# Kernel optimization log

Measured on AMD Instinct MI355X. Metric: run time of the kernel, lower is better.

## Reference

```python
import jax, jax.numpy as jnp
import numpy as np
from jax import lax

B, H, W, T, C = 2, 28, 28, 28, 192
WS = 7
NH = 6
HD = C // NH
N = WS ** 3
L = H * W * T

# static relative position index (matches torch buffer construction)
_coords = np.stack(np.meshgrid(np.arange(WS), np.arange(WS), np.arange(WS), indexing='ij'))  # (3,7,7,7)
_flat = _coords.reshape(3, -1)
_rel = (_flat[:, :, None] - _flat[:, None, :]).transpose(1, 2, 0).astype(np.int64)  # (N,N,3)
_rel[..., 0] += WS - 1; _rel[..., 1] += WS - 1; _rel[..., 2] += WS - 1
_rel[..., 0] *= (2 * WS - 1) ** 2
_rel[..., 1] *= (2 * WS - 1)
REL_IDX = jnp.asarray(_rel.sum(-1))  # (N,N)


def setup_inputs() -> dict:
    key = jax.random.key(0)
    ks = jax.random.split(key, 24)
    s = 0.02
    d = {
        'x': jax.random.normal(ks[0], (B, L, C), jnp.float32),
        'y': jax.random.normal(ks[1], (B, L, C), jnp.float32),
        'mask_matrix': jnp.zeros((64, N, N), jnp.float32),
        'norm1_g': jnp.ones((C,), jnp.float32),
        'norm1_b': jnp.zeros((C,), jnp.float32),
        'qkv_w': jax.random.normal(ks[2], (3 * C, C), jnp.float32) * s,
        'qkv_b': jnp.zeros((3 * C,), jnp.float32),
        'proj_w': jax.random.normal(ks[3], (C, C), jnp.float32) * s,
        'proj_b': jnp.zeros((C,), jnp.float32),
        'rpb_table': jax.random.normal(ks[4], ((2 * WS - 1) ** 3, NH), jnp.float32) * s,
        'norm2_g': jnp.ones((C,), jnp.float32),
        'norm2_b': jnp.zeros((C,), jnp.float32),
        'fc1_w': jax.random.normal(ks[5], (4 * C, C), jnp.float32) * s,
        'fc1_b': jnp.zeros((4 * C,), jnp.float32),
        'fc2_w': jax.random.normal(ks[6], (C, 4 * C), jnp.float32) * s,
        'fc2_b': jnp.zeros((C,), jnp.float32),
        'cab1_w': jax.random.normal(ks[7], (C // 3, C, 3, 3, 3), jnp.float32) * s,
        'cab1_b': jnp.zeros((C // 3,), jnp.float32),
        'cab2_w': jax.random.normal(ks[8], (C, C // 3, 3, 3, 3), jnp.float32) * s,
        'cab2_b': jnp.zeros((C,), jnp.float32),
        'ca1_w': jax.random.normal(ks[9], (C // 16, C), jnp.float32) * s,
        'ca1_b': jnp.zeros((C // 16,), jnp.float32),
        'ca2_w': jax.random.normal(ks[10], (C, C // 16), jnp.float32) * s,
        'ca2_b': jnp.zeros((C,), jnp.float32),
    }
    return d


def _ln(x, g, b, eps=1e-5):
    m = x.mean(-1, keepdims=True)
    v = jnp.mean(jnp.square(x - m), axis=-1, keepdims=True)
    return (x - m) * lax.rsqrt(v + eps) * g + b


def _conv3d(x, w, b, pad):
    out = lax.conv_general_dilated(x, w, (1, 1, 1), [(pad, pad)] * 3,
                                   dimension_numbers=('NCDHW', 'OIDHW', 'NCDHW'))
    return out + b[None, :, None, None, None]


def _cab(x5, cab1_w, cab1_b, cab2_w, cab2_b, ca1_w, ca1_b, ca2_w, ca2_b):
    # x5: (B,H,W,T,C) -> conv in NCDHW
    xc = x5.transpose(0, 4, 1, 2, 3)
    h = jax.nn.gelu(_conv3d(xc, cab1_w, cab1_b, 1), approximate=False)
    h = _conv3d(h, cab2_w, cab2_b, 1)
    # channel attention (adaptive avg pool to 1 + 1x1 convs)
    p = h.mean(axis=(2, 3, 4))                       # (B,C)
    a = jax.nn.relu(p @ ca1_w.T + ca1_b)
    a = jax.nn.sigmoid(a @ ca2_w.T + ca2_b)          # (B,C)
    h = h * a[:, :, None, None, None]
    return h.transpose(0, 2, 3, 4, 1).reshape(B, L, C)


def _window_partition(t):
    t = t.reshape(B, H // WS, WS, W // WS, WS, T // WS, WS, C)
    return t.transpose(0, 1, 3, 5, 2, 4, 6, 7).reshape(-1, N, C)


def _window_reverse(wins):
    t = wins.reshape(B, H // WS, W // WS, T // WS, WS, WS, WS, C)
    return t.transpose(0, 1, 4, 2, 5, 3, 6, 7).reshape(B, H, W, T, C)


def reference(x, y, mask_matrix, norm1_g, norm1_b, qkv_w, qkv_b, proj_w, proj_b,
              rpb_table, norm2_g, norm2_b, fc1_w, fc1_b, fc2_w, fc2_b,
              cab1_w, cab1_b, cab2_w, cab2_b, ca1_w, ca1_b, ca2_w, ca2_b):
    scale = HD ** (-0.5)
    shortcut = x
    xn = _ln(x, norm1_g, norm1_b)
    yn = _ln(y, norm1_g, norm1_b)
    x5 = xn.reshape(B, H, W, T, C)
    y5 = yn.reshape(B, H, W, T, C)

    conv_x = _cab(x5, cab1_w, cab1_b, cab2_w, cab2_b, ca1_w, ca1_b, ca2_w, ca2_b)

    # shift_size = (0,0,0): no roll, mask unused
    xw = _window_partition(x5)  # (B_, N, C)
    yw = _window_partition(y5)
    B_ = xw.shape[0]

    qkv_x = (xw @ qkv_w.T + qkv_b).reshape(B_, N, 3, NH, HD).transpose(2, 0, 3, 1, 4)
    qkv_y = (yw @ qkv_w.T + qkv_b).reshape(B_, N, 3, NH, HD).transpose(2, 0, 3, 1, 4)
    q = qkv_x[0] * scale          # (B_,NH,N,HD)
    k, v = qkv_y[1], qkv_y[2]

    attn = jnp.einsum('bhnd,bhmd->bhnm', q, k)
    rpb = rpb_table[REL_IDX.reshape(-1)].reshape(N, N, NH).transpose(2, 0, 1)  # (NH,N,N)
    attn = jax.nn.softmax(attn + rpb[None], axis=-1)
    out = jnp.einsum('bhnm,bhmd->bhnd', attn, v).transpose(0, 2, 1, 3).reshape(B_, N, C)
    out = out @ proj_w.T + proj_b

    attn_x = _window_reverse(out).reshape(B, L, C)

    x = shortcut + attn_x + conv_x
    h = _ln(x, norm2_g, norm2_b)
    h = jax.nn.gelu(h @ fc1_w.T + fc1_b, approximate=False) @ fc2_w.T + fc2_b
    return x + h
```

## Files before the change

### kernel.cpp

```cpp
#include <hip/hip_runtime.h>
#include <math.h>

constexpr int CB  = 2;
constexpr int CL  = 28 * 28 * 28;
constexpr int CC  = 192;
constexpr int CM  = CB * CL;

typedef unsigned short ushortT;
typedef __attribute__((ext_vector_type(8))) short bf16x8;
typedef __attribute__((ext_vector_type(4))) float f32x4;

__device__ __forceinline__ int xcd_swz(int lid, int total) {
  int q = total >> 3, r = total & 7;
  int x = lid & 7, s = lid >> 3;
  return (x < r ? x * (q + 1) : r * (q + 1) + (x - r) * q) + s;
}

__device__ __forceinline__ int tt_to_pos(int tt, int& b) {
  int bw = tt / 343;
  int n  = tt - bw * 343;
  b = bw >> 6;
  int wi = bw & 63;
  int n0 = n / 49, r = n - n0 * 49;
  int n1 = r / 7,  n2 = r - n1 * 7;
  int h = (wi >> 4) * 7 + n0;
  int w = ((wi >> 2) & 3) * 7 + n1;
  int t = (wi & 3) * 7 + n2;
  return (h * 28 + w) * 28 + t;
}

__device__ __forceinline__ float gelu_exact(float x) {
  return 0.5f * x * (1.0f + erff(x * 0.70710678118654752f));
}

__device__ __forceinline__ ushortT f2b(float x) {
  unsigned int u = __builtin_bit_cast(unsigned int, x);
  unsigned int r = (u + 0x7FFFu + ((u >> 16) & 1u)) >> 16;
  return (ushortT)r;
}
__device__ __forceinline__ float b2f(ushortT u) {
  return __builtin_bit_cast(float, (unsigned int)u << 16);
}

typedef __attribute__((address_space(3))) unsigned int lds_uint;
typedef const __attribute__((address_space(1))) unsigned int glb_uint;
__device__ __forceinline__ void stage16(const ushortT* g, ushortT* l) {
#if defined(__has_builtin) && __has_builtin(__builtin_amdgcn_global_load_lds)
  __builtin_amdgcn_global_load_lds((glb_uint*)g, (lds_uint*)l, 16, 0, 0);
#else
  *(uint4*)l = *(const uint4*)g;
#endif
}

__device__ __forceinline__ const bf16x8* ldsfrag(const ushortT* base, int row, int chunk) {
  return (const bf16x8*)((const char*)base + row * 128 + ((chunk ^ (row & 7)) << 4));
}

__global__ __launch_bounds__(256) void ln_prep_kernel(
    const float* __restrict__ in0, const float* __restrict__ in1,
    const float* __restrict__ g, const float* __restrict__ bb,
    ushortT* __restrict__ out0, ushortT* __restrict__ out1,
    const float* __restrict__ qkvw, const float* __restrict__ projw,
    const float* __restrict__ fc1w, const float* __restrict__ fc2w,
    const float* __restrict__ w1, const float* __restrict__ w2,
    const float* __restrict__ rpb,
    ushortT* qkvwb, ushortT* projwb, ushortT* fc1wb, ushortT* fc2wb,
    ushortT* w1rb, ushortT* w2rb, float4* rpb4) {
  int bid = blockIdx.x;
  if (bid < 21952) {
    int wave = threadIdx.x >> 6;
    int lane = threadIdx.x & 63;
    const float* in = (bid & 1) ? in1 : in0;
    ushortT* out = (bid & 1) ? out1 : out0;
    int row = (bid >> 1) * 4 + wave;
    const float* p = in + (size_t)row * CC;
    float v0 = p[lane], v1 = p[lane + 64], v2 = p[lane + 128];
    float s = v0 + v1 + v2;
    for (int o = 32; o; o >>= 1) s += __shfl_xor(s, o, 64);
    float mean = s * (1.0f / 192.0f);
    float d0 = v0 - mean, d1 = v1 - mean, d2 = v2 - mean;
    float qs = d0 * d0 + d1 * d1 + d2 * d2;
    for (int o = 32; o; o >>= 1) qs += __shfl_xor(qs, o, 64);
    float rs = rsqrtf(qs * (1.0f / 192.0f) + 1e-5f);
    ushortT* po = out + (size_t)row * CC;
    po[lane]       = f2b(d0 * rs * g[lane]       + bb[lane]);
    po[lane + 64]  = f2b(d1 * rs * g[lane + 64]  + bb[lane + 64]);
    po[lane + 128] = f2b(d2 * rs * g[lane + 128] + bb[lane + 128]);
    return;
  }
  int i = (bid - 21952) * 256 + threadIdx.x;
  if (i < 110592) { qkvwb[i] = f2b(qkvw[i]); return; }
  i -= 110592;
  if (i < 36864) { projwb[i] = f2b(projw[i]); return; }
  i -= 36864;
  if (i < 147456) { fc1wb[i] = f2b(fc1w[i]); return; }
  i -= 147456;
  if (i < 147456) { fc2wb[i] = f2b(fc2w[i]); return; }
  i -= 147456;
  if (i < 331776) {
    int o = i / 5184, r = i - o * 5184, tap = r / 192, c = r - tap * 192;
    w1rb[i] = f2b(w1[o * 5184 + c * 27 + tap]); return;
  }
  i -= 331776;
  if (i < 331776) {
    int o = i / 1728, r = i - o * 1728, tap = r / 64, c = r - tap * 64;
    w2rb[i] = f2b(w2[o * 1728 + c * 27 + tap]); return;
  }
  i -= 331776;
  if (i < 6 * 88 * 352) {
    int head = i / (88 * 352);
    int rem = i - head * 88 * 352;
    int qgrp = rem / 352, k = rem - qgrp * 352;
    float4 v = make_float4(0.f, 0.f, 0.f, 0.f);
    if (k < 343) {
      int b0 = k / 49, rb = k - b0 * 49; int b1 = rb / 7, b2 = rb - b1 * 7;
#pragma unroll
      for (int r = 0; r < 4; ++r) {
        int q = qgrp * 4 + r;
        if (q < 343) {
          int a0 = q / 49, ra = q - a0 * 49; int a1 = ra / 7, a2 = ra - a1 * 7;
          int ridx = ((a0 - b0 + 6) * 13 + (a1 - b1 + 6)) * 13 + (a2 - b2 + 6);
          (&v.x)[r] = rpb[ridx * 6 + head];
        }
      }
    }
    rpb4[i] = v;
  }
}

#define CORE_IDS \
  const int tid = threadIdx.x; \
  const int wave = tid >> 6, lane = tid & 63; \
  const int fr = lane & 15, g = lane >> 4; \
  const int wr = wave >> 1, wc = wave & 1;

#define ZERO_ACC(NF) \
  f32x4 acc[2][NF]; \
  _Pragma("unroll") \
  for (int m_ = 0; m_ < 2; ++m_) { \
    _Pragma("unroll") \
    for (int n_ = 0; n_ < NF; ++n_) acc[m_][n_] = (f32x4){0.f, 0.f, 0.f, 0.f}; \
  }

#define SETUP_A_ROWMAJOR(BASE, LDA) \
  const ushortT* pa[2]; ushortT* la[2]; \
  _Pragma("unroll") \
  for (int i = 0; i < 2; ++i) { \
    int slot = i * 256 + tid; int row_ = slot >> 3; \
    int cc8 = ((slot & 7) ^ (row_ & 7)) * 8; \
    pa[i] = (BASE) + (size_t)(blockIdx.x * 64 + row_) * (LDA) + cc8; \
    la[i] = Asl + slot * 8; \
  }

#define SETUP_A_WINDOWED(BASE) \
  const ushortT* pa[2]; ushortT* la[2]; \
  _Pragma("unroll") \
  for (int i = 0; i < 2; ++i) { \
    int slot = i * 256 + tid; int row_ = slot >> 3; \
    int cc8 = ((slot & 7) ^ (row_ & 7)) * 8; \
    int bq_; int pos_ = tt_to_pos(blockIdx.x * 64 + row_, bq_); \
    pa[i] = (BASE) + ((size_t)bq_ * CL + pos_) * CC + cc8; \
    la[i] = Asl + slot * 8; \
  }

#define SETUP_B(BASE, ROWOFF, LDB, NR) \
  const ushortT* pb[NR]; ushortT* lb[NR]; \
  _Pragma("unroll") \
  for (int i = 0; i < NR; ++i) { \
    int slot = i * 256 + tid; int row_ = slot >> 3; \
    int cc8 = ((slot & 7) ^ (row_ & 7)) * 8; \
    pb[i] = (BASE) + (size_t)((ROWOFF) + row_) * (LDB) + cc8; \
    lb[i] = Bsl + slot * 8; \
  }

#define STAGE_AB(NR) \
  _Pragma("unroll") \
  for (int i = 0; i < 2; ++i) { stage16(pa[i], la[i]); pa[i] += 64; } \
  _Pragma("unroll") \
  for (int i = 0; i < NR; ++i) { stage16(pb[i], lb[i]); pb[i] += 64; }

#define CORE_MFMA(NF) \
  __syncthreads(); \
  _Pragma("unroll") \
  for (int kk = 0; kk < 2; ++kk) { \
    bf16x8 a0 = *ldsfrag(Asl, wr * 32 + fr, kk * 4 + g); \
    bf16x8 a1 = *ldsfrag(Asl, wr * 32 + 16 + fr, kk * 4 + g); \
    _Pragma("unroll") \
    for (int n_ = 0; n_ < NF; ++n_) { \
      bf16x8 bn = *ldsfrag(Bsl, wc * ((NF) * 16) + n_ * 16 + fr, kk * 4 + g); \
      acc[0][n_] = __builtin_amdgcn_mfma_f32_16x16x32_bf16(a0, bn, acc[0][n_], 0, 0, 0); \
      acc[1][n_] = __builtin_amdgcn_mfma_f32_16x16x32_bf16(a1, bn, acc[1][n_], 0, 0, 0); \
    } \
  } \
  __syncthreads();

#define M128_ZERO \
  f32x4 acc[4][4]; \
  _Pragma("unroll") \
  for (int m_ = 0; m_ < 4; ++m_) \
    _Pragma("unroll") \
    for (int n_ = 0; n_ < 4; ++n_) acc[m_][n_] = (f32x4){0.f, 0.f, 0.f, 0.f};

#define M128_SETUP_A_ROWMAJOR(BASE, LDA) \
  const ushortT* pa[4]; ushortT* la[4]; \
  _Pragma("unroll") \
  for (int i = 0; i < 4; ++i) { \
    int slot = i * 256 + tid; int row_ = slot >> 3; \
    int cc8 = ((slot & 7) ^ (row_ & 7)) * 8; \
    pa[i] = (BASE) + (size_t)(mblk * 128 + row_) * (LDA) + cc8; \
    la[i] = Asl + slot * 8; \
  }

#define M128_SETUP_A_WINDOWED(BASE) \
  const ushortT* pa[4]; ushortT* la[4]; \
  _Pragma("unroll") \
  for (int i = 0; i < 4; ++i) { \
    int slot = i * 256 + tid; int row_ = slot >> 3; \
    int cc8 = ((slot & 7) ^ (row_ & 7)) * 8; \
    int bq_; int pos_ = tt_to_pos(mblk * 128 + row_, bq_); \
    pa[i] = (BASE) + ((size_t)bq_ * CL + pos_) * CC + cc8; \
    la[i] = Asl + slot * 8; \
  }

#define M128_SETUP_B(BASE, ROWOFF, LDB) \
  const ushortT* pb[4]; ushortT* lb[4]; \
  _Pragma("unroll") \
  for (int i = 0; i < 4; ++i) { \
    int slot = i * 256 + tid; int row_ = slot >> 3; \
    int cc8 = ((slot & 7) ^ (row_ & 7)) * 8; \
    pb[i] = (BASE) + (size_t)((ROWOFF) + row_) * (LDB) + cc8; \
    lb[i] = Bsl + slot * 8; \
  }

#define M128_STAGE \
  { _Pragma("unroll") \
    for (int i = 0; i < 4; ++i) { stage16(pa[i], la[i]); pa[i] += 64; } \
    _Pragma("unroll") \
    for (int i = 0; i < 4; ++i) { stage16(pb[i], lb[i]); pb[i] += 64; } }

#define M128_MFMA \
  { _Pragma("unroll") \
    for (int kk = 0; kk < 2; ++kk) { \
      bf16x8 am[4], bn[4]; \
      _Pragma("unroll") \
      for (int m_ = 0; m_ < 4; ++m_) am[m_] = *ldsfrag(Asl, wr * 64 + m_ * 16 + fr, kk * 4 + g); \
      _Pragma("unroll") \
      for (int n_ = 0; n_ < 4; ++n_) bn[n_] = *ldsfrag(Bsl, wc * 64 + n_ * 16 + fr, kk * 4 + g); \
      _Pragma("unroll") \
      for (int m_ = 0; m_ < 4; ++m_) \
        _Pragma("unroll") \
        for (int n_ = 0; n_ < 4; ++n_) \
          acc[m_][n_] = __builtin_amdgcn_mfma_f32_16x16x32_bf16(am[m_], bn[n_], acc[m_][n_], 0, 0, 0); \
    } }

#define M128_LOOP(KS) \
  _Pragma("unroll") \
  for (int ks = 0; ks < (KS); ++ks) { \
    M128_STAGE \
    __syncthreads(); \
    M128_MFMA \
    __syncthreads(); \
  }

__global__ __launch_bounds__(256) void gemm_q_n(const ushortT* __restrict__ xnb,
                                                const ushortT* __restrict__ qkvwb,
                                                const float* __restrict__ qkvb,
                                                ushortT* __restrict__ qout) {
  __shared__ alignas(16) ushortT Asl[64 * 64];
  __shared__ alignas(16) ushortT Bsl[192 * 64];
  CORE_IDS
  ZERO_ACC(6)
  SETUP_A_WINDOWED(xnb)
  SETUP_B(qkvwb, 0, 192, 6)
  for (int ks = 0; ks < 3; ++ks) {
    STAGE_AB(6)
    CORE_MFMA(6)
  }
#pragma unroll
  for (int n = 0; n < 6; ++n) {
    int jj = wc * 96 + n * 16 + fr;
    int head = jj >> 5, d = jj & 31;
    float bias = qkvb[jj];
#pragma unroll
    for (int m = 0; m < 2; ++m)
#pragma unroll
      for (int r = 0; r < 4; ++r) {
        int tt = blockIdx.x * 64 + wr * 32 + m * 16 + g * 4 + r;
        int bw = tt / 343, nn = tt - bw * 343;
        qout[(((size_t)bw * 6 + head) * 343 + nn) * 32 + d] =
            f2b((acc[m][n][r] + bias) * 0.17677669529663687f);
      }
  }
}

__global__ __launch_bounds__(256) void kv_128(const ushortT* __restrict__ ynb,
                                              const ushortT* __restrict__ qkvwb,
                                              const float* __restrict__ qkvb,
                                              ushortT* __restrict__ kout,
                                              ushortT* __restrict__ vout) {
  __shared__ alignas(16) ushortT Asl[8192];
  __shared__ alignas(16) ushortT Bsl[8192];
  CORE_IDS
  const int wid = xcd_swz(blockIdx.x, 343 * 3);
  const int mblk = wid / 3;
  const int jb = (wid - mblk * 3) * 128;
  M128_ZERO
  M128_SETUP_A_WINDOWED(ynb)
  M128_SETUP_B(qkvwb, 192 + jb, 192)
  M128_LOOP(3)
#pragma unroll
  for (int ni = 0; ni < 4; ++ni) {
    int jj = jb + wc * 64 + ni * 16 + fr;
    float bias = qkvb[192 + jj];
#pragma unroll
    for (int mi = 0; mi < 4; ++mi)
#pragma unroll
      for (int r = 0; r < 4; ++r) {
        int tt = mblk * 128 + wr * 64 + mi * 16 + g * 4 + r;
        int bw = tt / 343, nn = tt - bw * 343;
        float val = acc[mi][ni][r] + bias;
        if (jj < 192) {
          int head = jj >> 5, d = jj & 31;
          kout[(((size_t)bw * 6 + head) * 343 + nn) * 32 + d] = f2b(val);
        } else {
          int jv = jj - 192;
          int head = jv >> 5, d = jv & 31;
          vout[((size_t)bw * 6 + head) * 11264 + (size_t)d * 352 + nn] = f2b(val);
        }
      }
  }
}

template <int CIN, int COUTT, int MODE>
__global__ __launch_bounds__(256) void conv128(const ushortT* __restrict__ src,
                                               const ushortT* __restrict__ wrw,
                                               const float* __restrict__ bias,
                                               void* __restrict__ dst,
                                               float* __restrict__ part) {
  constexpr int KT = 27 * CIN;
  constexpr int KN = KT / 64;
  constexpr int NY = (MODE == 2) ? 4 : (COUTT / 64);
  constexpr int NBLK = 343 * NY;
  __shared__ alignas(16) ushortT Asl[8192];
  __shared__ alignas(16) ushortT Bsl[4096];
  const int tid = threadIdx.x;
  const int wave = tid >> 6, lane = tid & 63;
  const int fr = lane & 15, g = lane >> 4;
  const int wid = xcd_swz(blockIdx.x, NBLK);
  const int mblk = wid / NY;
  const int ysub = wid - mblk * NY;
  f32x4 acc[2][4];
#pragma unroll
  for (int m = 0; m < 2; ++m)
#pragma unroll
    for (int n = 0; n < 4; ++n) acc[m][n] = (f32x4){0.f, 0.f, 0.f, 0.f};

  const int kb = (MODE == 2) ? (ysub * KN) / 4 : 0;
  const int ke = (MODE == 2) ? ((ysub + 1) * KN) / 4 : KN;
  const int jbN = (MODE == 0) ? ysub * 64 : 0;

  const ushortT* srcb[4];
  ushortT* la[4];
  unsigned vmask[4];
#pragma unroll
  for (int i = 0; i < 4; ++i) {
    int slot = i * 256 + tid; int row_ = slot >> 3;
    int cc8 = ((slot & 7) ^ (row_ & 7)) * 8;
    int grow = mblk * 128 + row_;
    int bbq = grow / CL;
    int pos = grow - bbq * CL;
    int h = pos / 784, w = (pos / 28) % 28, t = pos % 28;
    unsigned vm = 0;
#pragma unroll
    for (int tap = 0; tap < 27; ++tap) {
      int dh = tap / 9 - 1, dw = (tap / 3) % 3 - 1, dt = tap % 3 - 1;
      bool ok = ((unsigned)(h + dh) < 28u) && ((unsigned)(w + dw) < 28u) &&
                ((unsigned)(t + dt) < 28u);
      vm |= (unsigned)ok << tap;
    }
    vmask[i] = vm;
    srcb[i] = src + ((size_t)bbq * CL + pos) * CIN + cc8;
    la[i] = Asl + slot * 8;
  }
  const ushortT* pb[2]; ushortT* lb[2];
#pragma unroll
  for (int i = 0; i < 2; ++i) {
    int slot = i * 256 + tid; int row_ = slot >> 3;
    int cc8 = ((slot & 7) ^ (row_ & 7)) * 8;
    pb[i] = wrw + (size_t)(jbN + row_) * KT + kb * 64 + cc8;
    lb[i] = Bsl + slot * 8;
  }

  auto loadA = [&](int ks, int i) -> uint4 {
    int tap, cb;
    if (CIN == 64) { tap = ks; cb = 0; }
    else           { tap = ks / 3; cb = (ks - tap * 3) * 64; }
    int off = ((tap / 9 - 1) * 784 + ((tap / 3) % 3 - 1) * 28 + (tap % 3 - 1)) * CIN + cb;
    uint4 v = make_uint4(0u, 0u, 0u, 0u);
    if ((vmask[i] >> tap) & 1u) v = *(const uint4*)(srcb[i] + off);
    return v;
  };

  uint4 vr[4];
#pragma unroll
  for (int i = 0; i < 4; ++i) vr[i] = loadA(kb, i);
  for (int ks = kb; ks < ke; ++ks) {
#pragma unroll
    for (int i = 0; i < 4; ++i) *(uint4*)la[i] = vr[i];
#pragma unroll
    for (int i = 0; i < 2; ++i) { stage16(pb[i], lb[i]); pb[i] += 64; }
    __syncthreads();
    bool more = (ks + 1 < ke);
    if (more) {
#pragma unroll
      for (int i = 0; i < 4; ++i) vr[i] = loadA(ks + 1, i);
    }
#pragma unroll
    for (int kk = 0; kk < 2; ++kk) {
      bf16x8 a0 = *ldsfrag(Asl, wave * 32 + fr, kk * 4 + g);
      bf16x8 a1 = *ldsfrag(Asl, wave * 32 + 16 + fr, kk * 4 + g);
#pragma unroll
      for (int n = 0; n < 4; ++n) {
        bf16x8 bn = *ldsfrag(Bsl, n * 16 + fr, kk * 4 + g);
        acc[0][n] = __builtin_amdgcn_mfma_f32_16x16x32_bf16(a0, bn, acc[0][n], 0, 0, 0);
        acc[1][n] = __builtin_amdgcn_mfma_f32_16x16x32_bf16(a1, bn, acc[1][n], 0, 0, 0);
      }
    }
    __syncthreads();
  }
  if (MODE == 2) {
#pragma unroll
    for (int n = 0; n < 4; ++n) {
      int jj = n * 16 + fr;
#pragma unroll
      for (int m = 0; m < 2; ++m)
#pragma unroll
        for (int r = 0; r < 4; ++r) {
          int grow = mblk * 128 + wave * 32 + m * 16 + g * 4 + r;
          ((float*)dst)[((size_t)ysub * CM + grow) * 64 + jj] = acc[m][n][r];
        }
    }
  } else {
    float* red = (float*)Asl;
#pragma unroll
    for (int n = 0; n < 4; ++n) {
      int jj = n * 16 + fr;
      float bs = bias[jbN + jj];
      float s0 = 0.f, s1 = 0.f;
#pragma unroll
      for (int m = 0; m < 2; ++m)
#pragma unroll
        for (int r = 0; r < 4; ++r) {
          int grow = mblk * 128 + wave * 32 + m * 16 + g * 4 + r;
          float v = acc[m][n][r] + bs;
          ((ushortT*)dst)[(size_t)grow * COUTT + jbN + jj] = f2b(v);
          if (grow < CL) s0 += v; else s1 += v;
        }
      s0 += __shfl_xor(s0, 16, 64); s0 += __shfl_xor(s0, 32, 64);
      s1 += __shfl_xor(s1, 16, 64); s1 += __shfl_xor(s1, 32, 64);
      if (g == 0) {
        red[((wave * 4 + n) * 16 + fr) * 2 + 0] = s0;
        red[((wave * 4 + n) * 16 + fr) * 2 + 1] = s1;
      }
    }
    __syncthreads();
    if (tid < 128) {
      int chl = tid >> 1, bsel = tid & 1;
      float s = 0.f;
#pragma unroll
      for (int wv = 0; wv < 4; ++wv)
        s += red[((wv * 4 + (chl >> 4)) * 16 + (chl & 15)) * 2 + bsel];
      if (s != 0.0f) atomicAdd(&part[bsel * 192 + jbN + chl], s);
    }
  }
}

__global__ __launch_bounds__(256) void comb1_kernel(const float* __restrict__ pc,
                                                    const float* __restrict__ b1,
                                                    ushortT* __restrict__ h1b) {
  size_t idx = ((size_t)blockIdx.x * 256 + threadIdx.x) * 4;
  float4 a = *(const float4*)(pc + idx);
  float4 b = *(const float4*)(pc + (size_t)CM * 64 + idx);
  float4 c = *(const float4*)(pc + (size_t)CM * 128 + idx);
  float4 d = *(const float4*)(pc + (size_t)CM * 192 + idx);
  int c0 = (int)(idx & 63);
  ushortT o0 = f2b(gelu_exact(a.x + b.x + c.x + d.x + b1[c0 + 0]));
  ushortT o1 = f2b(gelu_exact(a.y + b.y + c.y + d.y + b1[c0 + 1]));
  ushortT o2 = f2b(gelu_exact(a.z + b.z + c.z + d.z + b1[c0 + 2]));
  ushortT o3 = f2b(gelu_exact(a.w + b.w + c.w + d.w + b1[c0 + 3]));
  unsigned int w0 = (unsigned int)o0 | ((unsigned int)o1 << 16);
  unsigned int w1 = (unsigned int)o2 | ((unsigned int)o3 << 16);
  *(uint2*)&h1b[idx] = make_uint2(w0, w1);
}

constexpr int KP  = 36;
constexpr int VP  = 356;
constexpr int VP2 = 200;

__global__ __launch_bounds__(256) void attn_ca(const ushortT* __restrict__ qb,
                                               const ushortT* __restrict__ kb,
                                               const ushortT* __restrict__ vb,
                                               const float* __restrict__ rpb4,
                                               ushortT* __restrict__ aout,
                                               const float* __restrict__ part,
                                               const float* __restrict__ ca1w,
                                               const float* __restrict__ ca1b,
                                               const float* __restrict__ ca2w,
                                               const float* __restrict__ ca2b,
                                               float* __restrict__ av) {
  __shared__ ushortT Kl[352 * KP];
  __shared__ ushortT Vt[32 * VP];
  __shared__ ushortT Pl[64 * VP2];
  const int tid = threadIdx.x;

  if (blockIdx.x >= 1536) {
    int b = blockIdx.x - 1536;
    float* pl = (float*)Kl;
    float* hid = pl + 192;
    if (tid < 192) pl[tid] = part[b * 192 + tid] * (1.0f / (float)CL);
    __syncthreads();
    if (tid < 12) {
      float t = ca1b[tid];
      for (int i = 0; i < 192; ++i) t += ca1w[tid * 192 + i] * pl[i];
      hid[tid] = fmaxf(t, 0.0f);
    }
    __syncthreads();
    if (tid < 192) {
      float t = ca2b[tid];
#pragma unroll
      for (int j = 0; j < 12; ++j) t += ca2w[tid * 12 + j] * hid[j];
      av[b * 192 + tid] = 1.0f / (1.0f + __expf(-t));
    }
    return;
  }

  const int wave = tid >> 6, lane = tid & 63;
  const int fr = lane & 15, g = lane >> 4, fk = g * 8;
  const int wid = xcd_swz(blockIdx.x, 768 * 2);
  const int wh = wid >> 1;
  const int qhalf = wid & 1;
  const int bw = wh / 6, head = wh - bw * 6;
  const ushortT* kp = kb + (size_t)wh * 343 * 32;
  const ushortT* vp = vb + (size_t)wh * 11264;
  const ushortT* qp = qb + (size_t)wh * 343 * 32;
  const f32x4* bp4 = (const f32x4*)rpb4 + (size_t)head * 88 * 352;

  for (int c = tid; c < 1372; c += 256) {
    int key = c >> 2, part_ = c & 3;
    *(uint4*)&Kl[key * KP + part_ * 8] = *(const uint4*)(kp + (size_t)c * 8);
  }
  for (int c = tid; c < 1408; c += 256) {
    int d = c / 44, p = c - d * 44;
    *(uint4*)&Vt[d * VP + p * 8] = *(const uint4*)(vp + (size_t)c * 8);
  }
  __syncthreads();

  for (int qi = 0; qi < 3; ++qi) {
    const int q0 = (qhalf * 3 + qi) * 64;

    int qrow = q0 + wave * 16 + fr; if (qrow > 342) qrow = 342;
    bf16x8 aq = *(const bf16x8*)(qp + (size_t)qrow * 32 + fk);

    const int qgrp = (q0 + wave * 16) / 4 + g;
    f32x4 sc[22];
#pragma unroll
    for (int t = 0; t < 22; ++t) {
      f32x4 cini = bp4[(size_t)qgrp * 352 + t * 16 + fr];
      bf16x8 bk = *(const bf16x8*)&Kl[(t * 16 + fr) * KP + fk];
      sc[t] = __builtin_amdgcn_mfma_f32_16x16x32_bf16(aq, bk, cini, 0, 0, 0);
    }
    if (fr > 6) { sc[21][0] = -1e30f; sc[21][1] = -1e30f; sc[21][2] = -1e30f; sc[21][3] = -1e30f; }

    float rinv[4];
#pragma unroll
    for (int r = 0; r < 4; ++r) {
      float sum = 0.0f;
#pragma unroll
      for (int t = 0; t < 22; ++t) {
        float e = __expf(sc[t][r]);
        sc[t][r] = e;
        sum += e;
      }
      sum += __shfl_xor(sum, 1, 64); sum += __shfl_xor(sum, 2, 64);
      sum += __shfl_xor(sum, 4, 64); sum += __shfl_xor(sum, 8, 64);
      rinv[r] = 1.0f / sum;
    }

    f32x4 o0 = {0.f, 0.f, 0.f, 0.f}, o1 = {0.f, 0.f, 0.f, 0.f};

#pragma unroll
    for (int t = 0; t < 12; ++t)
#pragma unroll
      for (int r = 0; r < 4; ++r)
        Pl[(wave * 16 + g * 4 + r) * VP2 + t * 16 + fr] = f2b(sc[t][r]);
    asm volatile("s_waitcnt lgkmcnt(0)" ::: "memory");
#pragma unroll
    for (int s = 0; s < 6; ++s) {
      bf16x8 ap  = *(const bf16x8*)&Pl[(wave * 16 + fr) * VP2 + s * 32 + fk];
      bf16x8 bv0 = *(const bf16x8*)&Vt[fr * VP + s * 32 + fk];
      bf16x8 bv1 = *(const bf16x8*)&Vt[(16 + fr) * VP + s * 32 + fk];
      o0 = __builtin_amdgcn_mfma_f32_16x16x32_bf16(ap, bv0, o0, 0, 0, 0);
      o1 = __builtin_amdgcn_mfma_f32_16x16x32_bf16(ap, bv1, o1, 0, 0, 0);
    }
    asm volatile("s_waitcnt lgkmcnt(0)" ::: "memory");

#pragma unroll
    for (int t = 12; t < 22; ++t)
#pragma unroll
      for (int r = 0; r < 4; ++r)
        Pl[(wave * 16 + g * 4 + r) * VP2 + (t - 12) * 16 + fr] = f2b(sc[t][r]);
    asm volatile("s_waitcnt lgkmcnt(0)" ::: "memory");
#pragma unroll
    for (int s = 0; s < 5; ++s) {
      bf16x8 ap  = *(const bf16x8*)&Pl[(wave * 16 + fr) * VP2 + s * 32 + fk];
      bf16x8 bv0 = *(const bf16x8*)&Vt[fr * VP + 192 + s * 32 + fk];
      bf16x8 bv1 = *(const bf16x8*)&Vt[(16 + fr) * VP + 192 + s * 32 + fk];
      o0 = __builtin_amdgcn_mfma_f32_16x16x32_bf16(ap, bv0, o0, 0, 0, 0);
      o1 = __builtin_amdgcn_mfma_f32_16x16x32_bf16(ap, bv1, o1, 0, 0, 0);
    }
    asm volatile("s_waitcnt lgkmcnt(0)" ::: "memory");

#pragma unroll
    for (int r = 0; r < 4; ++r) {
      int q = q0 + wave * 16 + g * 4 + r;
      if (q < 343) {
        float ri = rinv[r];
        size_t base = ((size_t)bw * 343 + q) * 192 + head * 32;
        aout[base + fr]      = f2b(o0[r] * ri);
        aout[base + 16 + fr] = f2b(o1[r] * ri);
      }
    }
  }
}

__global__ __launch_bounds__(256) void proj_ln(const ushortT* __restrict__ attnrb,
                                               const ushortT* __restrict__ projwb,
                                               const float* __restrict__ projb,
                                               const float* __restrict__ x0,
                                               const ushortT* __restrict__ h2b,
                                               const float* __restrict__ cav,
                                               const float* __restrict__ n2g,
                                               const float* __restrict__ n2b,
                                               float* __restrict__ xout,
                                               ushortT* __restrict__ hlnb) {
  __shared__ alignas(16) ushortT Asl[64 * 64];
  __shared__ alignas(16) ushortT Bsl[192 * 64];
  CORE_IDS
  ZERO_ACC(6)
  SETUP_A_ROWMAJOR(attnrb, CC)
  SETUP_B(projwb, 0, 192, 6)
  for (int ks = 0; ks < 3; ++ks) {
    STAGE_AB(6)
    CORE_MFMA(6)
  }
  size_t sbase[2][4];
#pragma unroll
  for (int m = 0; m < 2; ++m)
#pragma unroll
    for (int r = 0; r < 4; ++r) {
      int tt = blockIdx.x * 64 + wr * 32 + m * 16 + g * 4 + r;
      int bq_;
      int pos_ = tt_to_pos(tt, bq_);
      size_t base = ((size_t)bq_ * CL + pos_) * CC;
      sbase[m][r] = base;
#pragma unroll
      for (int n = 0; n < 6; ++n) {
        int jj = wc * 96 + n * 16 + fr;
        size_t addr = base + jj;
        float v = x0[addr] + acc[m][n][r] + projb[jj] + b2f(h2b[addr]) * cav[bq_ * 192 + jj];
        acc[m][n][r] = v;
        xout[addr] = v;
      }
    }
  float* stats = (float*)Asl;
#pragma unroll
  for (int m = 0; m < 2; ++m)
#pragma unroll
    for (int r = 0; r < 4; ++r) {
      float ps = 0.f, ps2 = 0.f;
#pragma unroll
      for (int n = 0; n < 6; ++n) { float v = acc[m][n][r]; ps += v; ps2 += v * v; }
      ps  += __shfl_xor(ps, 1, 64);  ps2 += __shfl_xor(ps2, 1, 64);
      ps  += __shfl_xor(ps, 2, 64);  ps2 += __shfl_xor(ps2, 2, 64);
      ps  += __shfl_xor(ps, 4, 64);  ps2 += __shfl_xor(ps2, 4, 64);
      ps  += __shfl_xor(ps, 8, 64);  ps2 += __shfl_xor(ps2, 8, 64);
      if (fr == 0) {
        int lrow = wr * 32 + m * 16 + g * 4 + r;
        stats[lrow * 4 + wc * 2]     = ps;
        stats[lrow * 4 + wc * 2 + 1] = ps2;
      }
    }
  __syncthreads();
#pragma unroll
  for (int m = 0; m < 2; ++m)
#pragma unroll
    for (int r = 0; r < 4; ++r) {
      int lrow = wr * 32 + m * 16 + g * 4 + r;
      float s  = stats[lrow * 4]     + stats[lrow * 4 + 2];
      float s2 = stats[lrow * 4 + 1] + stats[lrow * 4 + 3];
      float mean = s * (1.0f / 192.0f);
      float var  = s2 * (1.0f / 192.0f) - mean * mean;
      float rs = rsqrtf(var + 1e-5f);
      ushortT* po = hlnb + sbase[m][r];
#pragma unroll
      for (int n = 0; n < 6; ++n) {
        int jj = wc * 96 + n * 16 + fr;
        po[jj] = f2b((acc[m][n][r] - mean) * rs * n2g[jj] + n2b[jj]);
      }
    }
}

__global__ __launch_bounds__(256) void fc1_128(const ushortT* __restrict__ hlnb,
                                               const ushortT* __restrict__ fc1wb,
                                               const float* __restrict__ fc1b,
                                               ushortT* __restrict__ hidb) {
  __shared__ alignas(16) ushortT Asl[8192];
  __shared__ alignas(16) ushortT Bsl[8192];
  CORE_IDS
  const int wid = xcd_swz(blockIdx.x, 343 * 6);
  const int mblk = wid / 6;
  const int jb = (wid - mblk * 6) * 128;
  M128_ZERO
  M128_SETUP_A_ROWMAJOR(hlnb, CC)
  M128_SETUP_B(fc1wb, jb, 192)
  M128_LOOP(3)
#pragma unroll
  for (int ni = 0; ni < 4; ++ni) {
    int jj = jb + wc * 64 + ni * 16 + fr;
    float bs = fc1b[jj];
#pragma unroll
    for (int mi = 0; mi < 4; ++mi)
#pragma unroll
      for (int r = 0; r < 4; ++r) {
        int grow = mblk * 128 + wr * 64 + mi * 16 + g * 4 + r;
        hidb[(size_t)grow * 768 + jj] = f2b(gelu_exact(acc[mi][ni][r] + bs));
      }
  }
}

__global__ __launch_bounds__(256) void fc2_n(const ushortT* __restrict__ hidb,
                                             const ushortT* __restrict__ fc2wb,
                                             const float* __restrict__ fc2b,
                                             const float* __restrict__ xout,
                                             float* __restrict__ out) {
  __shared__ alignas(16) ushortT Asl[64 * 64];
  __shared__ alignas(16) ushortT Bsl[192 * 64];
  CORE_IDS
  ZERO_ACC(6)
  SETUP_A_ROWMAJOR(hidb, 768)
  SETUP_B(fc2wb, 0, 768, 6)
  for (int ks = 0; ks < 12; ++ks) {
    STAGE_AB(6)
    CORE_MFMA(6)
  }
#pragma unroll
  for (int n = 0; n < 6; ++n) {
    int jj = wc * 96 + n * 16 + fr;
    float bs = fc2b[jj];
#pragma unroll
    for (int m = 0; m < 2; ++m)
#pragma unroll
      for (int r = 0; r < 4; ++r) {
        int grow = blockIdx.x * 64 + wr * 32 + m * 16 + g * 4 + r;
        size_t addr = (size_t)grow * CC + jj;
        out[addr] = xout[addr] + acc[m][n][r] + bs;
      }
  }
}

extern "C" void kernel_launch(void* const* d_in, const int* in_sizes, int n_in,
                              void* d_out, int out_size, void* d_ws, size_t ws_size,
                              hipStream_t stream) {
  const float* x     = (const float*)d_in[0];
  const float* y     = (const float*)d_in[1];
  const float* n1g   = (const float*)d_in[3];
  const float* n1b   = (const float*)d_in[4];
  const float* qkvw  = (const float*)d_in[5];
  const float* qkvb  = (const float*)d_in[6];
  const float* projw = (const float*)d_in[7];
  const float* projb = (const float*)d_in[8];
  const float* rpb   = (const float*)d_in[9];
  const float* n2g   = (const float*)d_in[10];
  const float* n2b   = (const float*)d_in[11];
  const float* fc1w  = (const float*)d_in[12];
  const float* fc1b  = (const float*)d_in[13];
  const float* fc2w  = (const float*)d_in[14];
  const float* fc2b  = (const float*)d_in[15];
  const float* w1    = (const float*)d_in[16];
  const float* b1    = (const float*)d_in[17];
  const float* w2    = (const float*)d_in[18];
  const float* b2    = (const float*)d_in[19];
  const float* ca1w  = (const float*)d_in[20];
  const float* ca1b  = (const float*)d_in[21];
  const float* ca2w  = (const float*)d_in[22];
  const float* ca2b  = (const float*)d_in[23];

  char* W = (char*)d_ws;
  float* out = (float*)d_out;

  ushortT* xnb  = (ushortT*)(W + 0);
  ushortT* ynb  = (ushortT*)(W + 16859136);
  ushortT* qbb  = (ushortT*)(W + 33718272);
  ushortT* kbb  = (ushortT*)(W + 50577408);
  ushortT* vbb  = (ushortT*)(W + 67436544);
  ushortT* h1b  = (ushortT*)(W + 84738048);
  ushortT* h2b  = (ushortT*)(W + 90357760);
  float*   xo   = (float*)(W + 124076032);
  char*    SM   = W + 157794304;
  ushortT* qkvwb  = (ushortT*)(SM);
  ushortT* projwb = (ushortT*)(SM + 221184);
  ushortT* fc1wb  = (ushortT*)(SM + 294912);
  ushortT* fc2wb  = (ushortT*)(SM + 589824);
  ushortT* w1rb   = (ushortT*)(SM + 884736);
  ushortT* w2rb   = (ushortT*)(SM + 1548288);
  float*   rpb4   = (float*)(SM + 2211840);
  float*   av     = (float*)(SM + 5185536);
  float*   part   = (float*)(SM + 5187072);
  float*   pc1    = (float*)(SM + 5319168);
  ushortT* attnrb = xnb;
  ushortT* hlnb   = ynb;
  ushortT* hidb   = (ushortT*)(W + 33718272);

  hipMemsetAsync(part, 0, 2 * 192 * sizeof(float), stream);

  ln_prep_kernel<<<21952 + 5046, 256, 0, stream>>>(
      x, y, n1g, n1b, xnb, ynb,
      qkvw, projw, fc1w, fc2w, w1, w2, rpb,
      qkvwb, projwb, fc1wb, fc2wb, w1rb, w2rb, (float4*)rpb4);

  gemm_q_n<<<686, 256, 0, stream>>>(xnb, qkvwb, qkvb, qbb);
  kv_128<<<343 * 3, 256, 0, stream>>>(ynb, qkvwb, qkvb, kbb, vbb);

  conv128<192, 64, 2><<<343 * 4, 256, 0, stream>>>(xnb, w1rb, b1, pc1, nullptr);
  comb1_kernel<<<2744, 256, 0, stream>>>(pc1, b1, h1b);
  conv128<64, 192, 0><<<343 * 3, 256, 0, stream>>>(h1b, w2rb, b2, h2b, part);

  attn_ca<<<1538, 256, 0, stream>>>(qbb, kbb, vbb, rpb4, attnrb,
                                    part, ca1w, ca1b, ca2w, ca2b, av);

  proj_ln<<<686, 256, 0, stream>>>(attnrb, projwb, projb, x, h2b, av, n2g, n2b, xo, hlnb);

  fc1_128<<<343 * 6, 256, 0, stream>>>(hlnb, fc1wb, fc1b, hidb);
  fc2_n<<<686, 256, 0, stream>>>(hidb, fc2wb, fc2b, xo, out);
}
```

Measured before the change: 398.7 us.

## Merge independent kernels into horizontally fused launches sharing a block range

Combines the Q GEMM, KV GEMM and first conv into a single launch, dispatching each block by its index, and likewise merges the second conv with the windowed attention. The channel-attention MLP moves out of the attention kernel into a small separate kernel. The aim is fewer launch gaps and tail-wave idle time, since independent work can fill the GPU concurrently. The cost is that the merged kernels take the largest shared-memory footprint (72KB for conv2attn), so the conv blocks may run at lower occupancy.

```diff
diff --git a/kernel.cpp b/kernel.cpp
--- a/kernel.cpp
+++ b/kernel.cpp
@@ -142,23 +142,23 @@
     for (int n_ = 0; n_ < NF; ++n_) acc[m_][n_] = (f32x4){0.f, 0.f, 0.f, 0.f}; \
   }
 
-#define SETUP_A_ROWMAJOR(BASE, LDA) \
+#define SETUP_A_ROWMAJOR(BASE, LDA, BX) \
   const ushortT* pa[2]; ushortT* la[2]; \
   _Pragma("unroll") \
   for (int i = 0; i < 2; ++i) { \
     int slot = i * 256 + tid; int row_ = slot >> 3; \
     int cc8 = ((slot & 7) ^ (row_ & 7)) * 8; \
-    pa[i] = (BASE) + (size_t)(blockIdx.x * 64 + row_) * (LDA) + cc8; \
+    pa[i] = (BASE) + (size_t)((BX) * 64 + row_) * (LDA) + cc8; \
     la[i] = Asl + slot * 8; \
   }
 
-#define SETUP_A_WINDOWED(BASE) \
+#define SETUP_A_WINDOWED(BASE, BX) \
   const ushortT* pa[2]; ushortT* la[2]; \
   _Pragma("unroll") \
   for (int i = 0; i < 2; ++i) { \
     int slot = i * 256 + tid; int row_ = slot >> 3; \
     int cc8 = ((slot & 7) ^ (row_ & 7)) * 8; \
-    int bq_; int pos_ = tt_to_pos(blockIdx.x * 64 + row_, bq_); \
+    int bq_; int pos_ = tt_to_pos((BX) * 64 + row_, bq_); \
     pa[i] = (BASE) + ((size_t)bq_ * CL + pos_) * CC + cc8; \
     la[i] = Asl + slot * 8; \
   }
@@ -262,15 +262,14 @@
     __syncthreads(); \
   }
 
-__global__ __launch_bounds__(256) void gemm_q_n(const ushortT* __restrict__ xnb,
-                                                const ushortT* __restrict__ qkvwb,
-                                                const float* __restrict__ qkvb,
-                                                ushortT* __restrict__ qout) {
-  __shared__ alignas(16) ushortT Asl[64 * 64];
-  __shared__ alignas(16) ushortT Bsl[192 * 64];
+__device__ __forceinline__ void gemmq_body(int bx, ushortT* Asl, ushortT* Bsl,
+                                           const ushortT* __restrict__ xnb,
+                                           const ushortT* __restrict__ qkvwb,
+                                           const float* __restrict__ qkvb,
+                                           ushortT* __restrict__ qout) {
   CORE_IDS
   ZERO_ACC(6)
-  SETUP_A_WINDOWED(xnb)
+  SETUP_A_WINDOWED(xnb, bx)
   SETUP_B(qkvwb, 0, 192, 6)
   for (int ks = 0; ks < 3; ++ks) {
     STAGE_AB(6)
@@ -285,7 +284,7 @@
     for (int m = 0; m < 2; ++m)
 #pragma unroll
       for (int r = 0; r < 4; ++r) {
-        int tt = blockIdx.x * 64 + wr * 32 + m * 16 + g * 4 + r;
+        int tt = bx * 64 + wr * 32 + m * 16 + g * 4 + r;
         int bw = tt / 343, nn = tt - bw * 343;
         qout[(((size_t)bw * 6 + head) * 343 + nn) * 32 + d] =
             f2b((acc[m][n][r] + bias) * 0.17677669529663687f);
@@ -293,15 +292,14 @@
   }
 }
 
-__global__ __launch_bounds__(256) void kv_128(const ushortT* __restrict__ ynb,
-                                              const ushortT* __restrict__ qkvwb,
-                                              const float* __restrict__ qkvb,
-                                              ushortT* __restrict__ kout,
-                                              ushortT* __restrict__ vout) {
-  __shared__ alignas(16) ushortT Asl[8192];
-  __shared__ alignas(16) ushortT Bsl[8192];
+__device__ __forceinline__ void kv_body(int bx, ushortT* Asl, ushortT* Bsl,
+                                        const ushortT* __restrict__ ynb,
+                                        const ushortT* __restrict__ qkvwb,
+                                        const float* __restrict__ qkvb,
+                                        ushortT* __restrict__ kout,
+                                        ushortT* __restrict__ vout) {
   CORE_IDS
-  const int wid = xcd_swz(blockIdx.x, 343 * 3);
+  const int wid = xcd_swz(bx, 343 * 3);
   const int mblk = wid / 3;
   const int jb = (wid - mblk * 3) * 128;
   M128_ZERO
@@ -332,21 +330,20 @@
 }
 
 template <int CIN, int COUTT, int MODE>
-__global__ __launch_bounds__(256) void conv128(const ushortT* __restrict__ src,
-                                               const ushortT* __restrict__ wrw,
-                                               const float* __restrict__ bias,
-                                               void* __restrict__ dst,
-                                               float* __restrict__ part) {
+__device__ __forceinline__ void conv_body(int bx, ushortT* Asl, ushortT* Bsl,
+                                          const ushortT* __restrict__ src,
+                                          const ushortT* __restrict__ wrw,
+                                          const float* __restrict__ bias,
+                                          void* __restrict__ dst,
+                                          float* __restrict__ part) {
   constexpr int KT = 27 * CIN;
   constexpr int KN = KT / 64;
   constexpr int NY = (MODE == 2) ? 4 : (COUTT / 64);
   constexpr int NBLK = 343 * NY;
-  __shared__ alignas(16) ushortT Asl[8192];
-  __shared__ alignas(16) ushortT Bsl[4096];
   const int tid = threadIdx.x;
   const int wave = tid >> 6, lane = tid & 63;
   const int fr = lane & 15, g = lane >> 4;
-  const int wid = xcd_swz(blockIdx.x, NBLK);
+  const int wid = xcd_swz(bx, NBLK);
   const int mblk = wid / NY;
   const int ysub = wid - mblk * NY;
   f32x4 acc[2][4];
@@ -472,6 +469,136 @@
         s += red[((wv * 4 + (chl >> 4)) * 16 + (chl & 15)) * 2 + bsel];
       if (s != 0.0f) atomicAdd(&part[bsel * 192 + jbN + chl], s);
     }
+  }
+}
+
+constexpr int KP  = 36;
+constexpr int VP  = 356;
+constexpr int VP2 = 200;
+
+__device__ __forceinline__ void attn_body(int bx, ushortT* Kl, ushortT* Vt, ushortT* Pl,
+                                          const ushortT* __restrict__ qb,
+                                          const ushortT* __restrict__ kb,
+                                          const ushortT* __restrict__ vb,
+                                          const float* __restrict__ rpb4,
+                                          ushortT* __restrict__ aout) {
+  const int tid = threadIdx.x;
+  const int wave = tid >> 6, lane = tid & 63;
+  const int fr = lane & 15, g = lane >> 4, fk = g * 8;
+  const int wid = xcd_swz(bx, 768 * 2);
+  const int wh = wid >> 1;
+  const int qhalf = wid & 1;
+  const int bw = wh / 6, head = wh - bw * 6;
+  const ushortT* kp = kb + (size_t)wh * 343 * 32;
+  const ushortT* vp = vb + (size_t)wh * 11264;
+  const ushortT* qp = qb + (size_t)wh * 343 * 32;
+  const f32x4* bp4 = (const f32x4*)rpb4 + (size_t)head * 88 * 352;
+
+  for (int c = tid; c < 1372; c += 256) {
+    int key = c >> 2, pp = c & 3;
+    *(uint4*)&Kl[key * KP + pp * 8] = *(const uint4*)(kp + (size_t)c * 8);
+  }
+  for (int c = tid; c < 1408; c += 256) {
+    int d = c / 44, p = c - d * 44;
+    *(uint4*)&Vt[d * VP + p * 8] = *(const uint4*)(vp + (size_t)c * 8);
+  }
+  __syncthreads();
+
+  for (int qi = 0; qi < 3; ++qi) {
+    const int q0 = (qhalf * 3 + qi) * 64;
+
+    int qrow = q0 + wave * 16 + fr; if (qrow > 342) qrow = 342;
+    bf16x8 aq = *(const bf16x8*)(qp + (size_t)qrow * 32 + fk);
+
+    const int qgrp = (q0 + wave * 16) / 4 + g;
+    f32x4 sc[22];
+#pragma unroll
+    for (int t = 0; t < 22; ++t) {
+      f32x4 cini = bp4[(size_t)qgrp * 352 + t * 16 + fr];
+      bf16x8 bk = *(const bf16x8*)&Kl[(t * 16 + fr) * KP + fk];
+      sc[t] = __builtin_amdgcn_mfma_f32_16x16x32_bf16(aq, bk, cini, 0, 0, 0);
+    }
+    if (fr > 6) { sc[21][0] = -1e30f; sc[21][1] = -1e30f; sc[21][2] = -1e30f; sc[21][3] = -1e30f; }
+
+    float rinv[4];
+#pragma unroll
+    for (int r = 0; r < 4; ++r) {
+      float sum = 0.0f;
+#pragma unroll
+      for (int t = 0; t < 22; ++t) {
+        float e = __expf(sc[t][r]);
+        sc[t][r] = e;
+        sum += e;
+      }
+      sum += __shfl_xor(sum, 1, 64); sum += __shfl_xor(sum, 2, 64);
+      sum += __shfl_xor(sum, 4, 64); sum += __shfl_xor(sum, 8, 64);
+      rinv[r] = 1.0f / sum;
+    }
+
+    f32x4 o0 = {0.f, 0.f, 0.f, 0.f}, o1 = {0.f, 0.f, 0.f, 0.f};
+
+#pragma unroll
+    for (int t = 0; t < 12; ++t)
+#pragma unroll
+      for (int r = 0; r < 4; ++r)
+        Pl[(wave * 16 + g * 4 + r) * VP2 + t * 16 + fr] = f2b(sc[t][r]);
+    asm volatile("s_waitcnt lgkmcnt(0)" ::: "memory");
+#pragma unroll
+    for (int s = 0; s < 6; ++s) {
+      bf16x8 ap  = *(const bf16x8*)&Pl[(wave * 16 + fr) * VP2 + s * 32 + fk];
+      bf16x8 bv0 = *(const bf16x8*)&Vt[fr * VP + s * 32 + fk];
+      bf16x8 bv1 = *(const bf16x8*)&Vt[(16 + fr) * VP + s * 32 + fk];
+      o0 = __builtin_amdgcn_mfma_f32_16x16x32_bf16(ap, bv0, o0, 0, 0, 0);
+      o1 = __builtin_amdgcn_mfma_f32_16x16x32_bf16(ap, bv1, o1, 0, 0, 0);
+    }
+    asm volatile("s_waitcnt lgkmcnt(0)" ::: "memory");
+
+#pragma unroll
+    for (int t = 12; t < 22; ++t)
+#pragma unroll
+      for (int r = 0; r < 4; ++r)
+        Pl[(wave * 16 + g * 4 + r) * VP2 + (t - 12) * 16 + fr] = f2b(sc[t][r]);
+    asm volatile("s_waitcnt lgkmcnt(0)" ::: "memory");
+#pragma unroll
+    for (int s = 0; s < 5; ++s) {
+      bf16x8 ap  = *(const bf16x8*)&Pl[(wave * 16 + fr) * VP2 + s * 32 + fk];
+      bf16x8 bv0 = *(const bf16x8*)&Vt[fr * VP + 192 + s * 32 + fk];
+      bf16x8 bv1 = *(const bf16x8*)&Vt[(16 + fr) * VP + 192 + s * 32 + fk];
+      o0 = __builtin_amdgcn_mfma_f32_16x16x32_bf16(ap, bv0, o0, 0, 0, 0);
+      o1 = __builtin_amdgcn_mfma_f32_16x16x32_bf16(ap, bv1, o1, 0, 0, 0);
+    }
+    asm volatile("s_waitcnt lgkmcnt(0)" ::: "memory");
+
+#pragma unroll
+    for (int r = 0; r < 4; ++r) {
+      int q = q0 + wave * 16 + g * 4 + r;
+      if (q < 343) {
+        float ri = rinv[r];
+        size_t base = ((size_t)bw * 343 + q) * 192 + head * 32;
+        aout[base + fr]      = f2b(o0[r] * ri);
+        aout[base + 16 + fr] = f2b(o1[r] * ri);
+      }
+    }
+  }
+}
+
+__global__ __launch_bounds__(256) void phaseA(const ushortT* __restrict__ xnb,
+                                              const ushortT* __restrict__ ynb,
+                                              const ushortT* __restrict__ qkvwb,
+                                              const float* __restrict__ qkvb,
+                                              const ushortT* __restrict__ w1rb,
+                                              ushortT* __restrict__ qout,
+                                              ushortT* __restrict__ kout,
+                                              ushortT* __restrict__ vout,
+                                              float* __restrict__ pc1) {
+  __shared__ alignas(16) ushortT SH[16384];
+  const int bid = blockIdx.x;
+  if (bid < 1372) {
+    conv_body<192, 64, 2>(bid, SH, SH + 8192, xnb, w1rb, nullptr, pc1, nullptr);
+  } else if (bid < 2401) {
+    kv_body(bid - 1372, SH, SH + 8192, ynb, qkvwb, qkvb, kout, vout);
+  } else {
+    gemmq_body(bid - 2401, SH, SH + 4096, xnb, qkvwb, qkvb, qout);
   }
 }
 
@@ -493,144 +620,46 @@
   *(uint2*)&h1b[idx] = make_uint2(w0, w1);
 }
 
-constexpr int KP  = 36;
-constexpr int VP  = 356;
-constexpr int VP2 = 200;
-
-__global__ __launch_bounds__(256) void attn_ca(const ushortT* __restrict__ qb,
-                                               const ushortT* __restrict__ kb,
-                                               const ushortT* __restrict__ vb,
-                                               const float* __restrict__ rpb4,
-                                               ushortT* __restrict__ aout,
-                                               const float* __restrict__ part,
-                                               const float* __restrict__ ca1w,
-                                               const float* __restrict__ ca1b,
-                                               const float* __restrict__ ca2w,
-                                               const float* __restrict__ ca2b,
-                                               float* __restrict__ av) {
-  __shared__ ushortT Kl[352 * KP];
-  __shared__ ushortT Vt[32 * VP];
-  __shared__ ushortT Pl[64 * VP2];
-  const int tid = threadIdx.x;
-
-  if (blockIdx.x >= 1536) {
-    int b = blockIdx.x - 1536;
-    float* pl = (float*)Kl;
-    float* hid = pl + 192;
-    if (tid < 192) pl[tid] = part[b * 192 + tid] * (1.0f / (float)CL);
-    __syncthreads();
-    if (tid < 12) {
-      float t = ca1b[tid];
-      for (int i = 0; i < 192; ++i) t += ca1w[tid * 192 + i] * pl[i];
-      hid[tid] = fmaxf(t, 0.0f);
-    }
-    __syncthreads();
-    if (tid < 192) {
-      float t = ca2b[tid];
-#pragma unroll
-      for (int j = 0; j < 12; ++j) t += ca2w[tid * 12 + j] * hid[j];
-      av[b * 192 + tid] = 1.0f / (1.0f + __expf(-t));
-    }
-    return;
-  }
-
-  const int wave = tid >> 6, lane = tid & 63;
-  const int fr = lane & 15, g = lane >> 4, fk = g * 8;
-  const int wid = xcd_swz(blockIdx.x, 768 * 2);
-  const int wh = wid >> 1;
-  const int qhalf = wid & 1;
-  const int bw = wh / 6, head = wh - bw * 6;
-  const ushortT* kp = kb + (size_t)wh * 343 * 32;
-  const ushortT* vp = vb + (size_t)wh * 11264;
-  const ushortT* qp = qb + (size_t)wh * 343 * 32;
-  const f32x4* bp4 = (const f32x4*)rpb4 + (size_t)head * 88 * 352;
-
-  for (int c = tid; c < 1372; c += 256) {
-    int key = c >> 2, part_ = c & 3;
-    *(uint4*)&Kl[key * KP + part_ * 8] = *(const uint4*)(kp + (size_t)c * 8);
-  }
-  for (int c = tid; c < 1408; c += 256) {
-    int d = c / 44, p = c - d * 44;
-    *(uint4*)&Vt[d * VP + p * 8] = *(const uint4*)(vp + (size_t)c * 8);
-  }
+__global__ __launch_bounds__(256) void conv2attn(const ushortT* __restrict__ h1b,
+                                                 const ushortT* __restrict__ w2rb,
+                                                 const float* __restrict__ b2,
+                                                 ushortT* __restrict__ h2b,
+                                                 float* __restrict__ part,
+                                                 const ushortT* __restrict__ qb,
+                                                 const ushortT* __restrict__ kb,
+                                                 const ushortT* __restrict__ vb,
+                                                 const float* __restrict__ rpb4,
+                                                 ushortT* __restrict__ aout) {
+  __shared__ alignas(16) ushortT SH[36864];
+  const int bid = blockIdx.x;
+  if (bid < 1029) {
+    conv_body<64, 192, 0>(bid, SH, SH + 8192, h1b, w2rb, b2, h2b, part);
+  } else {
+    attn_body(bid - 1029, SH, SH + 12672, SH + 24064, qb, kb, vb, rpb4, aout);
+  }
+}
+
+__global__ __launch_bounds__(192) void ca_kernel(const float* __restrict__ part,
+                                                 const float* __restrict__ ca1w,
+                                                 const float* __restrict__ ca1b,
+                                                 const float* __restrict__ ca2w,
+                                                 const float* __restrict__ ca2b,
+                                                 float* __restrict__ av) {
+  __shared__ float pl[192];
+  __shared__ float hid[12];
+  int c = threadIdx.x, b = blockIdx.x;
+  pl[c] = part[b * 192 + c] * (1.0f / (float)CL);
   __syncthreads();
-
-  for (int qi = 0; qi < 3; ++qi) {
-    const int q0 = (qhalf * 3 + qi) * 64;
-
-    int qrow = q0 + wave * 16 + fr; if (qrow > 342) qrow = 342;
-    bf16x8 aq = *(const bf16x8*)(qp + (size_t)qrow * 32 + fk);
-
-    const int qgrp = (q0 + wave * 16) / 4 + g;
-    f32x4 sc[22];
-#pragma unroll
-    for (int t = 0; t < 22; ++t) {
-      f32x4 cini = bp4[(size_t)qgrp * 352 + t * 16 + fr];
-      bf16x8 bk = *(const bf16x8*)&Kl[(t * 16 + fr) * KP + fk];
-      sc[t] = __builtin_amdgcn_mfma_f32_16x16x32_bf16(aq, bk, cini, 0, 0, 0);
-    }
-    if (fr > 6) { sc[21][0] = -1e30f; sc[21][1] = -1e30f; sc[21][2] = -1e30f; sc[21][3] = -1e30f; }
-
-    float rinv[4];
-#pragma unroll
-    for (int r = 0; r < 4; ++r) {
-      float sum = 0.0f;
-#pragma unroll
-      for (int t = 0; t < 22; ++t) {
-        float e = __expf(sc[t][r]);
-        sc[t][r] = e;
-        sum += e;
-      }
-      sum += __shfl_xor(sum, 1, 64); sum += __shfl_xor(sum, 2, 64);
-      sum += __shfl_xor(sum, 4, 64); sum += __shfl_xor(sum, 8, 64);
-      rinv[r] = 1.0f / sum;
-    }
-
-    f32x4 o0 = {0.f, 0.f, 0.f, 0.f}, o1 = {0.f, 0.f, 0.f, 0.f};
-
-#pragma unroll
-    for (int t = 0; t < 12; ++t)
-#pragma unroll
-      for (int r = 0; r < 4; ++r)
-        Pl[(wave * 16 + g * 4 + r) * VP2 + t * 16 + fr] = f2b(sc[t][r]);
-    asm volatile("s_waitcnt lgkmcnt(0)" ::: "memory");
-#pragma unroll
-    for (int s = 0; s < 6; ++s) {
-      bf16x8 ap  = *(const bf16x8*)&Pl[(wave * 16 + fr) * VP2 + s * 32 + fk];
-      bf16x8 bv0 = *(const bf16x8*)&Vt[fr * VP + s * 32 + fk];
-      bf16x8 bv1 = *(const bf16x8*)&Vt[(16 + fr) * VP + s * 32 + fk];
-      o0 = __builtin_amdgcn_mfma_f32_16x16x32_bf16(ap, bv0, o0, 0, 0, 0);
-      o1 = __builtin_amdgcn_mfma_f32_16x16x32_bf16(ap, bv1, o1, 0, 0, 0);
-    }
-    asm volatile("s_waitcnt lgkmcnt(0)" ::: "memory");
-
-#pragma unroll
-    for (int t = 12; t < 22; ++t)
-#pragma unroll
-      for (int r = 0; r < 4; ++r)
-        Pl[(wave * 16 + g * 4 + r) * VP2 + (t - 12) * 16 + fr] = f2b(sc[t][r]);
-    asm volatile("s_waitcnt lgkmcnt(0)" ::: "memory");
-#pragma unroll
-    for (int s = 0; s < 5; ++s) {
-      bf16x8 ap  = *(const bf16x8*)&Pl[(wave * 16 + fr) * VP2 + s * 32 + fk];
-      bf16x8 bv0 = *(const bf16x8*)&Vt[fr * VP + 192 + s * 32 + fk];
-      bf16x8 bv1 = *(const bf16x8*)&Vt[(16 + fr) * VP + 192 + s * 32 + fk];
-      o0 = __builtin_amdgcn_mfma_f32_16x16x32_bf16(ap, bv0, o0, 0, 0, 0);
-      o1 = __builtin_amdgcn_mfma_f32_16x16x32_bf16(ap, bv1, o1, 0, 0, 0);
-    }
-    asm volatile("s_waitcnt lgkmcnt(0)" ::: "memory");
-
-#pragma unroll
-    for (int r = 0; r < 4; ++r) {
-      int q = q0 + wave * 16 + g * 4 + r;
-      if (q < 343) {
-        float ri = rinv[r];
-        size_t base = ((size_t)bw * 343 + q) * 192 + head * 32;
-        aout[base + fr]      = f2b(o0[r] * ri);
-        aout[base + 16 + fr] = f2b(o1[r] * ri);
-      }
-    }
-  }
+  if (c < 12) {
+    float t = ca1b[c];
+    for (int i = 0; i < 192; ++i) t += ca1w[c * 192 + i] * pl[i];
+    hid[c] = fmaxf(t, 0.0f);
+  }
+  __syncthreads();
+  float t = ca2b[c];
+#pragma unroll
+  for (int j = 0; j < 12; ++j) t += ca2w[c * 12 + j] * hid[j];
+  av[b * 192 + c] = 1.0f / (1.0f + __expf(-t));
 }
 
 __global__ __launch_bounds__(256) void proj_ln(const ushortT* __restrict__ attnrb,
@@ -646,8 +675,9 @@
   __shared__ alignas(16) ushortT Asl[64 * 64];
   __shared__ alignas(16) ushortT Bsl[192 * 64];
   CORE_IDS
+  const int bx = blockIdx.x;
   ZERO_ACC(6)
-  SETUP_A_ROWMAJOR(attnrb, CC)
+  SETUP_A_ROWMAJOR(attnrb, CC, bx)
   SETUP_B(projwb, 0, 192, 6)
   for (int ks = 0; ks < 3; ++ks) {
     STAGE_AB(6)
@@ -658,7 +688,7 @@
   for (int m = 0; m < 2; ++m)
 #pragma unroll
     for (int r = 0; r < 4; ++r) {
-      int tt = blockIdx.x * 64 + wr * 32 + m * 16 + g * 4 + r;
+      int tt = bx * 64 + wr * 32 + m * 16 + g * 4 + r;
       int bq_;
       int pos_ = tt_to_pos(tt, bq_);
       size_t base = ((size_t)bq_ * CL + pos_) * CC;
@@ -746,8 +776,9 @@
   __shared__ alignas(16) ushortT Asl[64 * 64];
   __shared__ alignas(16) ushortT Bsl[192 * 64];
   CORE_IDS
+  const int bx = blockIdx.x;
   ZERO_ACC(6)
-  SETUP_A_ROWMAJOR(hidb, 768)
+  SETUP_A_ROWMAJOR(hidb, 768, bx)
   SETUP_B(fc2wb, 0, 768, 6)
   for (int ks = 0; ks < 12; ++ks) {
     STAGE_AB(6)
@@ -761,7 +792,7 @@
     for (int m = 0; m < 2; ++m)
 #pragma unroll
       for (int r = 0; r < 4; ++r) {
-        int grow = blockIdx.x * 64 + wr * 32 + m * 16 + g * 4 + r;
+        int grow = bx * 64 + wr * 32 + m * 16 + g * 4 + r;
         size_t addr = (size_t)grow * CC + jj;
         out[addr] = xout[addr] + acc[m][n][r] + bs;
       }
@@ -828,15 +859,15 @@
       qkvw, projw, fc1w, fc2w, w1, w2, rpb,
       qkvwb, projwb, fc1wb, fc2wb, w1rb, w2rb, (float4*)rpb4);
 
-  gemm_q_n<<<686, 256, 0, stream>>>(xnb, qkvwb, qkvb, qbb);
-  kv_128<<<343 * 3, 256, 0, stream>>>(ynb, qkvwb, qkvb, kbb, vbb);
-
-  conv128<192, 64, 2><<<343 * 4, 256, 0, stream>>>(xnb, w1rb, b1, pc1, nullptr);
+  phaseA<<<1372 + 1029 + 686, 256, 0, stream>>>(xnb, ynb, qkvwb, qkvb, w1rb,
+                                                qbb, kbb, vbb, pc1);
+
   comb1_kernel<<<2744, 256, 0, stream>>>(pc1, b1, h1b);
-  conv128<64, 192, 0><<<343 * 3, 256, 0, stream>>>(h1b, w2rb, b2, h2b, part);
-
-  attn_ca<<<1538, 256, 0, stream>>>(qbb, kbb, vbb, rpb4, attnrb,
-                                    part, ca1w, ca1b, ca2w, ca2b, av);
+
+  conv2attn<<<1029 + 1536, 256, 0, stream>>>(h1b, w2rb, b2, h2b, part,
+                                             qbb, kbb, vbb, rpb4, attnrb);
+
+  ca_kernel<<<2, 192, 0, stream>>>(part, ca1w, ca1b, ca2w, ca2b, av);
 
   proj_ln<<<686, 256, 0, stream>>>(attnrb, projwb, projb, x, h2b, av, n2g, n2b, xo, hlnb);
 
```

Measured after the change: 465.5 us. +16.7%, slower.
